# Kernel optimization log

Hardware: AMD Instinct MI355X
Metric: run time of the kernel (lower is better)

The kernel has to match this reference:

```python
import jax, jax.numpy as jnp
import numpy as np

D_MODEL, HEADS, D_FF = 768, 12, 3072
D_K = D_MODEL // HEADS
EPS = 1e-6


def _norm(x, alpha, bias):
    # NormalizationLayer: scalar alpha/bias, torch.std is unbiased (ddof=1)
    mean = jnp.mean(x, axis=-1, keepdims=True)
    std = jnp.std(x, axis=-1, ddof=1, keepdims=True)
    return alpha * (x - mean) / (std + EPS) + bias


def setup_inputs() -> dict:
    key = jax.random.key(0)
    ks = jax.random.split(key, 16)
    B, S = 2, 4096
    x = jax.random.normal(ks[0], (B, S, D_MODEL), dtype=jnp.float32)
    mask = jax.random.randint(ks[1], (B, 1, 1, S), 0, 2, dtype=jnp.int32)
    w = lambda k, o, i: (jax.random.normal(k, (o, i), dtype=jnp.float32) * 0.02)
    return {
        "x": x, "mask": mask,
        "wq": w(ks[2], D_MODEL, D_MODEL), "bq": jnp.zeros((D_MODEL,), jnp.float32),
        "wk": w(ks[3], D_MODEL, D_MODEL), "bk": jnp.zeros((D_MODEL,), jnp.float32),
        "wv": w(ks[4], D_MODEL, D_MODEL), "bv": jnp.zeros((D_MODEL,), jnp.float32),
        "wo": w(ks[5], D_MODEL, D_MODEL), "bo": jnp.zeros((D_MODEL,), jnp.float32),
        "w1": w(ks[6], D_FF, D_MODEL), "b1": jnp.zeros((D_FF,), jnp.float32),
        "w2": w(ks[7], D_MODEL, D_FF), "b2": jnp.zeros((D_MODEL,), jnp.float32),
        "alpha1": jnp.ones((1,), jnp.float32), "beta1": jnp.ones((1,), jnp.float32),
        "alpha2": jnp.ones((1,), jnp.float32), "beta2": jnp.ones((1,), jnp.float32),
    }


def reference(x, mask, wq, bq, wk, bk, wv, bv, wo, bo, w1, b1, w2, b2,
              alpha1, beta1, alpha2, beta2):
    B, S, _ = x.shape

    # --- residual connection 0: pre-norm + self-attention ---
    h = _norm(x, alpha1, beta1)
    q = (h @ wq.T + bq).reshape(B, S, HEADS, D_K).transpose(0, 2, 1, 3)  # [B,H,S,dk]
    k = (h @ wk.T + bk).reshape(B, S, HEADS, D_K).transpose(0, 2, 1, 3)
    v = (h @ wv.T + bv).reshape(B, S, HEADS, D_K).transpose(0, 2, 1, 3)
    scores = jnp.einsum('bhqd,bhkd->bhqk', q, k) / jnp.sqrt(jnp.float32(D_K))
    scores = jnp.where(mask == 0, jnp.float32(-1e9), scores)
    attn = jax.nn.softmax(scores, axis=-1)
    ctx = jnp.einsum('bhqk,bhkd->bhqd', attn, v)
    ctx = ctx.transpose(0, 2, 1, 3).reshape(B, S, D_MODEL)
    x = x + (ctx @ wo.T + bo)

    # --- residual connection 1: pre-norm + FFN ---
    h = _norm(x, alpha2, beta2)
    ff = jax.nn.relu(h @ w1.T + b1) @ w2.T + b2
    return x + ff
```

## Files before the change

kernel.cpp:

```cpp
#include <hip/hip_runtime.h>
#include <hip/hip_bf16.h>
#include <math.h>


typedef __hip_bfloat16 bf16;
typedef short short8 __attribute__((ext_vector_type(8)));
typedef short short4v __attribute__((ext_vector_type(4)));
typedef float f32x4 __attribute__((ext_vector_type(4)));

#define MFMA(A, B, C) __builtin_amdgcn_mfma_f32_16x16x32_bf16(A, B, C, 0, 0, 0)

#if __has_builtin(__builtin_amdgcn_exp2f)
#define EXP2(x) __builtin_amdgcn_exp2f(x)
#else
#define EXP2(x) exp2f(x)
#endif

#define PSWAP32(a, b) asm("v_permlane32_swap_b32 %0, %1" : "+v"(a), "+v"(b))
#define PSWAP16(a, b) asm("v_permlane16_swap_b32 %0, %1" : "+v"(a), "+v"(b))

__device__ __forceinline__ unsigned cvt_pk(float lo, float hi) {
  unsigned r;
  asm("v_cvt_pk_bf16_f32 %0, %1, %2" : "=v"(r) : "v"(lo), "v"(hi));
  return r;
}

__device__ __forceinline__ void gl_lds16(const void* g, void* l) {
  __builtin_amdgcn_global_load_lds(
      (__attribute__((address_space(1))) void*)g,
      (__attribute__((address_space(3))) void*)l, 16, 0, 0);
}

__device__ __forceinline__ short f2b(float f) {
  bf16 h = __float2bfloat16(f);
  return *reinterpret_cast<short*>(&h);
}

__global__ __launch_bounds__(256)
void prep_all(const float* __restrict__ wq, const float* __restrict__ wk,
              const float* __restrict__ wv, const float* __restrict__ wo,
              const float* __restrict__ w1, const float* __restrict__ w2,
              const float* __restrict__ bq, const float* __restrict__ bk,
              const float* __restrict__ bv, const int* __restrict__ mask,
              bf16* __restrict__ wqkvb, bf16* __restrict__ wob,
              bf16* __restrict__ w1b, bf16* __restrict__ w2b,
              float* __restrict__ bqkv,
              int* __restrict__ pos_g, int* __restrict__ nch_g,
              bf16* __restrict__ kc, bf16* __restrict__ vtc)
{
  const int t = threadIdx.x;
  if (blockIdx.x < 2) {
    const int b = blockIdx.x;
    const int* mb = mask + b * 4096;
    __shared__ int lsum[256];
    int loc = 0;
    int mv[16];
#pragma unroll
    for (int j = 0; j < 16; j++) { mv[j] = mb[t * 16 + j] ? 1 : 0; loc += mv[j]; }
    lsum[t] = loc;
    __syncthreads();
    for (int off = 1; off < 256; off <<= 1) {
      int v = (t >= off) ? lsum[t - off] : 0;
      __syncthreads();
      lsum[t] += v;
      __syncthreads();
    }
    const int nvalid = lsum[255];
    int base = lsum[t] - loc;
#pragma unroll
    for (int j = 0; j < 16; j++) {
      pos_g[b * 4096 + t * 16 + j] = mv[j] ? base : -1;
      if (mv[j]) base++;
    }
    const int npad = (nvalid + 63) & ~63;
    if (t == 0) { nch_g[b * 2] = npad >> 6; nch_g[b * 2 + 1] = npad - nvalid; }
    const int npv = npad - nvalid;
    if (npv > 0) {
      const int krows = 12 * npv;
      const short8 z = {};
      for (int task = t; task < krows * 8; task += 256) {
        const int rr = task >> 3, cc = task & 7;
        const int hh = rr / npv, r = nvalid + rr % npv;
        *(short8*)&kc[(((long)(b * 12 + hh) * 4096) + r) * 64 + cc * 8] = z;
      }
      const int vrows = 12 * 64;
      for (int task = t; task < vrows * npv; task += 256) {
        const int row = task / npv, j = nvalid + task % npv;
        const int hh = row >> 6, d = row & 63;
        vtc[((long)((b * 12 + hh) * 64 + d)) * 4096 + j] = __float2bfloat16(0.f);
      }
    }
    return;
  }
  const int i = (blockIdx.x - 2) * 256 + t;
  const int W = 147456;
  const int F = 589824;
  const float* src; bf16* dst; int off;
  if (i < W)          { src = wq; dst = wqkvb;           off = i; }
  else if (i < 2*W)   { src = wk; dst = wqkvb + 589824;  off = i - W; }
  else if (i < 3*W)   { src = wv; dst = wqkvb + 1179648; off = i - 2*W; }
  else if (i < 4*W)   { src = wo; dst = wob;             off = i - 3*W; }
  else if (i < 4*W+F) { src = w1; dst = w1b;             off = i - 4*W; }
  else                { src = w2; dst = w2b;             off = i - 4*W - F; }
  float4 v = ((const float4*)src)[off];
  short4v o;
  o.x = f2b(v.x); o.y = f2b(v.y); o.z = f2b(v.z); o.w = f2b(v.w);
  ((short4v*)dst)[off] = o;
  if (i < 2304)
    bqkv[i] = (i < 768) ? bq[i] : (i < 1536 ? bk[i - 768] : bv[i - 1536]);
}

template<typename INT>
__global__ __launch_bounds__(256)
void ln_kernel(const INT* __restrict__ x, bf16* __restrict__ out,
               const float* __restrict__ alpha, const float* __restrict__ beta)
{
  const int row = blockIdx.x;
  const long base = (long)row * 768;
  const int t = threadIdx.x;
  float v[3]; float s = 0.f, ss = 0.f;
#pragma unroll
  for (int i = 0; i < 3; i++) {
    v[i] = (float)x[base + t + i * 256];
    s += v[i]; ss += v[i] * v[i];
  }
#pragma unroll
  for (int off = 32; off > 0; off >>= 1) {
    s  += __shfl_down(s, off);
    ss += __shfl_down(ss, off);
  }
  __shared__ float red[8];
  __shared__ float stats[2];
  const int w = t >> 6;
  if ((t & 63) == 0) { red[w] = s; red[4 + w] = ss; }
  __syncthreads();
  if (t == 0) {
    float S  = red[0] + red[1] + red[2] + red[3];
    float SS = red[4] + red[5] + red[6] + red[7];
    float mean = S * (1.f / 768.f);
    float var = fmaxf((SS - 768.f * mean * mean) * (1.f / 767.f), 0.f);
    stats[0] = mean;
    stats[1] = 1.f / (sqrtf(var) + 1e-6f);
  }
  __syncthreads();
  const float mean = stats[0], rinv = stats[1];
  const float a = alpha[0], b = beta[0];
#pragma unroll
  for (int i = 0; i < 3; i++)
    out[base + t + i * 256] = __float2bfloat16(a * (v[i] - mean) * rinv + b);
}

template<int MODE, int TM, typename RT, typename OUTT>
__global__ __launch_bounds__(256)
void gemm_bt(const bf16* __restrict__ A, const bf16* __restrict__ W,
             const float* __restrict__ bias, const RT* __restrict__ R,
             OUTT* __restrict__ Cout, int M, int N, int K)
{
  constexpr int MI = TM / 32;
  __shared__ __align__(16) bf16 sA[2][TM * 32];
  __shared__ __align__(16) bf16 sB[2][128 * 32];
  const int t = threadIdx.x;
  const int w = t >> 6, lane = t & 63;
  const int lr = lane & 15, quad = lane >> 4;
  const int tm = blockIdx.x * TM, tn = blockIdx.y * 128;
  const int wm = (w >> 1) * (MI * 16), wn = (w & 1) * 64;

  const int srow = w * 16 + (lane >> 2);
  const int sq = lane & 3;
  const int scol = (sq ^ ((srow >> 1) & 3)) * 8;
  const int soff = srow * 32 + sq * 8;
  const bf16* Ap = A + (long)(tm + srow) * K + scol;
  const bf16* Wp = W + (long)(tn + srow) * K + scol;
  const long half = (long)64 * K;

  auto stage = [&](int kb, int bi) {
    gl_lds16(Ap + kb, &sA[bi][soff]);
    if (TM == 128) gl_lds16(Ap + kb + half, &sA[bi][soff + 64 * 32]);
    gl_lds16(Wp + kb, &sB[bi][soff]);
    gl_lds16(Wp + kb + half, &sB[bi][soff + 64 * 32]);
  };

  const int cQ = (quad ^ ((lr >> 1) & 3)) * 8;

  f32x4 acc[MI][4] = {};

  stage(0, 0);
  int bi = 0;
  for (int kb = 0; kb < K; kb += 32, bi ^= 1) {
    __syncthreads();
    if (kb + 32 < K) stage(kb + 32, bi ^ 1);
    const bf16* sAb = sA[bi];
    const bf16* sBb = sB[bi];
    short8 af[MI], bfr[4];
#pragma unroll
    for (int i = 0; i < MI; i++)
      af[i] = *(const short8*)&sAb[(wm + i * 16 + lr) * 32 + cQ];
#pragma unroll
    for (int j = 0; j < 4; j++)
      bfr[j] = *(const short8*)&sBb[(wn + j * 16 + lr) * 32 + cQ];
#pragma unroll
    for (int i = 0; i < MI; i++)
#pragma unroll
      for (int j = 0; j < 4; j++)
        acc[i][j] = MFMA(af[i], bfr[j], acc[i][j]);
  }

#pragma unroll
  for (int i = 0; i < MI; i++) {
#pragma unroll
    for (int j = 0; j < 4; j++) {
      const int col = tn + wn + j * 16 + lr;
      const float bv = bias[col];
#pragma unroll
      for (int r = 0; r < 4; r++) {
        const int m = tm + wm + i * 16 + quad * 4 + r;
        float vv = acc[i][j][r] + bv;
        if (MODE == 1) vv = fmaxf(vv, 0.f);
        if (MODE == 4) vv += (float)R[(long)m * N + col];
        Cout[(long)m * N + col] = (OUTT)vv;
      }
    }
  }
}

__global__ __launch_bounds__(256)
void gemm_qkv(const bf16* __restrict__ A, const bf16* __restrict__ W,
              const float* __restrict__ bias, const int* __restrict__ pos_g,
              bf16* __restrict__ Qo, bf16* __restrict__ Kc, bf16* __restrict__ Vtc)
{
  const int K = 768;
  __shared__ __align__(16) bf16 sA[2][128 * 32];
  __shared__ __align__(16) bf16 sB[2][128 * 32];
  const int t = threadIdx.x;
  const int w = t >> 6, lane = t & 63;
  const int lr = lane & 15, quad = lane >> 4;
  const int tm = blockIdx.x * 128, tn = blockIdx.y * 128;
  const int wm = (w >> 1) * 64, wn = (w & 1) * 64;

  const int srow = w * 16 + (lane >> 2);
  const int sq = lane & 3;
  const int scol = (sq ^ ((srow >> 1) & 3)) * 8;
  const int soff = srow * 32 + sq * 8;
  const bf16* Ap = A + (long)(tm + srow) * K + scol;
  const bf16* Wp = W + (long)(tn + srow) * K + scol;
  const long half = (long)64 * K;

  auto stage = [&](int kb, int bi) {
    gl_lds16(Ap + kb, &sA[bi][soff]);
    gl_lds16(Ap + kb + half, &sA[bi][soff + 64 * 32]);
    gl_lds16(Wp + kb, &sB[bi][soff]);
    gl_lds16(Wp + kb + half, &sB[bi][soff + 64 * 32]);
  };

  const int cQ = (quad ^ ((lr >> 1) & 3)) * 8;

  f32x4 acc[4][4] = {};

  stage(0, 0);
  int bi = 0;
  for (int kb = 0; kb < K; kb += 32, bi ^= 1) {
    __syncthreads();
    if (kb + 32 < K) stage(kb + 32, bi ^ 1);
    const bf16* sAb = sA[bi];
    const bf16* sBb = sB[bi];
    short8 af[4], bfr[4];
#pragma unroll
    for (int i = 0; i < 4; i++)
      af[i] = *(const short8*)&sAb[(wm + i * 16 + lr) * 32 + cQ];
#pragma unroll
    for (int j = 0; j < 4; j++)
      bfr[j] = *(const short8*)&sBb[(wn + j * 16 + lr) * 32 + cQ];
#pragma unroll
    for (int i = 0; i < 4; i++)
#pragma unroll
      for (int j = 0; j < 4; j++)
        acc[i][j] = MFMA(af[i], bfr[j], acc[i][j]);
  }

  const int region = (tn >= 1536) ? 2 : (tn >= 768 ? 1 : 0);
#pragma unroll
  for (int i = 0; i < 4; i++) {
#pragma unroll
    for (int j = 0; j < 4; j++) {
      const int col = tn + wn + j * 16 + lr;
      const int c768 = col - region * 768;
      const int hh = c768 >> 6, d = c768 & 63;
      const float bv = bias[col];
#pragma unroll
      for (int r = 0; r < 4; r++) {
        const int m = tm + wm + i * 16 + quad * 4 + r;
        const int bb = m >> 12, sdx = m & 4095;
        float vv = acc[i][j][r] + bv;
        if (region == 0) {
          vv *= 0.18033688011112042f;
          Qo[((long)(bb * 12 + hh) * 4096 + sdx) * 64 + d] = __float2bfloat16(vv);
        } else {
          const int p_ = pos_g[bb * 4096 + sdx];
          if (p_ >= 0) {
            if (region == 1)
              Kc[((long)(bb * 12 + hh) * 4096 + p_) * 64 + d] = __float2bfloat16(vv);
            else
              Vtc[((long)(bb * 12 + hh) * 64 + d) * 4096 + p_] = __float2bfloat16(vv);
          }
        }
      }
    }
  }
}

__global__ __launch_bounds__(256)
void attn_kernel(const bf16* __restrict__ Q, const bf16* __restrict__ Kg,
                 const bf16* __restrict__ Vt,
                 const int* __restrict__ nch_g, bf16* __restrict__ ctx)
{
  __shared__ __align__(16) bf16 sK[2][64 * 64];
  __shared__ __align__(16) bf16 sV[2][64 * 64];

  const int t = threadIdx.x, w = t >> 6, lane = t & 63;
  const int lr = lane & 15, quad = lane >> 4;
  const int bh = blockIdx.y, b = bh / 12, hh = bh % 12;
  const int qb = blockIdx.x * 128 + w * 32;
  const long bh_s = (long)bh * 4096;
  const int nch = nch_g[b * 2];
  const int npv = nch_g[b * 2 + 1];

  short8 qf[2][2];
#pragma unroll
  for (int qt = 0; qt < 2; qt++) {
    const bf16* qp = Q + (bh_s + qb + qt * 16 + lr) * 64 + quad * 8;
    qf[qt][0] = *(const short8*)qp;
    qf[qt][1] = *(const short8*)(qp + 32);
  }

  short8 ones;
#pragma unroll
  for (int i = 0; i < 8; i++) ones[i] = (short)0x3F80;

  const int rA = w * 16 + (lane >> 3), rB = rA + 8;
  const int c8 = lane & 7;
  const bf16* kA = Kg + (bh_s + rA) * 64 + ((c8 ^ (rA & 7)) << 3);
  const bf16* kB = Kg + (bh_s + rB) * 64 + ((c8 ^ (rB & 7)) << 3);
  const bf16* vA = Vt + ((long)bh * 64 + rA) * 4096 + ((c8 ^ (rA & 7)) << 3);
  const bf16* vB = Vt + ((long)bh * 64 + rB) * 4096 + ((c8 ^ (rB & 7)) << 3);
  const int ldsA = (w * 16) * 64 + lane * 8;
  const int ldsB = ldsA + 8 * 64;

  const int cA = (quad * 8) ^ ((lr & 7) << 3);

  f32x4 lacc[2] = {};
  f32x4 Ot[4][2] = {};

  auto stage = [&](int kc, int buf) {
    gl_lds16(kA + (long)kc * 64, &sK[buf][ldsA]);
    gl_lds16(kB + (long)kc * 64, &sK[buf][ldsB]);
    gl_lds16(vA + kc, &sV[buf][ldsA]);
    gl_lds16(vB + kc, &sV[buf][ldsB]);
  };

  auto compute = [&](int buf) {
    const bf16* Kb = sK[buf];
    const bf16* Vb = sV[buf];
    f32x4 st[4][2] = {};
    __builtin_amdgcn_s_setprio(1);
#pragma unroll
    for (int kt = 0; kt < 4; kt++) {
      const int rowb = (kt * 16 + lr) * 64;
      short8 kfa = *(const short8*)&Kb[rowb + cA];
      short8 kfb = *(const short8*)&Kb[rowb + (cA ^ 32)];
      st[kt][0] = MFMA(kfa, qf[0][0], st[kt][0]);
      st[kt][0] = MFMA(kfb, qf[0][1], st[kt][0]);
      st[kt][1] = MFMA(kfa, qf[1][0], st[kt][1]);
      st[kt][1] = MFMA(kfb, qf[1][1], st[kt][1]);
    }
    __builtin_amdgcn_s_setprio(0);

    short8 pf[2][2];
#pragma unroll
    for (int qt = 0; qt < 2; qt++) {
      float p[4][4];
#pragma unroll
      for (int kt = 0; kt < 4; kt++)
#pragma unroll
        for (int r = 0; r < 4; r++)
          p[kt][r] = EXP2(st[kt][qt][r]);
      unsigned u00 = cvt_pk(p[0][0], p[0][1]), u01 = cvt_pk(p[0][2], p[0][3]);
      unsigned u10 = cvt_pk(p[1][0], p[1][1]), u11 = cvt_pk(p[1][2], p[1][3]);
      unsigned u20 = cvt_pk(p[2][0], p[2][1]), u21 = cvt_pk(p[2][2], p[2][3]);
      unsigned u30 = cvt_pk(p[3][0], p[3][1]), u31 = cvt_pk(p[3][2], p[3][3]);
      PSWAP32(u00, u10); PSWAP32(u01, u11);
      PSWAP32(u20, u30); PSWAP32(u21, u31);
      PSWAP16(u00, u10); PSWAP16(u01, u11);
      PSWAP16(u20, u30); PSWAP16(u21, u31);
      union { unsigned u[4]; short8 s8; } fa, fb;
      fa.u[0] = u00; fa.u[1] = u01; fa.u[2] = u10; fa.u[3] = u11;
      fb.u[0] = u20; fb.u[1] = u21; fb.u[2] = u30; fb.u[3] = u31;
      pf[qt][0] = fa.s8;
      pf[qt][1] = fb.s8;
    }

    __builtin_amdgcn_s_setprio(1);
#pragma unroll
    for (int dt = 0; dt < 4; dt++) {
      const int rowb = (dt * 16 + lr) * 64;
      short8 vfa = *(const short8*)&Vb[rowb + cA];
      short8 vfb = *(const short8*)&Vb[rowb + (cA ^ 32)];
      Ot[dt][0] = MFMA(vfa, pf[0][0], Ot[dt][0]);
      Ot[dt][0] = MFMA(vfb, pf[0][1], Ot[dt][0]);
      Ot[dt][1] = MFMA(vfa, pf[1][0], Ot[dt][1]);
      Ot[dt][1] = MFMA(vfb, pf[1][1], Ot[dt][1]);
    }
    lacc[0] = MFMA(ones, pf[0][0], lacc[0]);
    lacc[0] = MFMA(ones, pf[0][1], lacc[0]);
    lacc[1] = MFMA(ones, pf[1][0], lacc[1]);
    lacc[1] = MFMA(ones, pf[1][1], lacc[1]);
    __builtin_amdgcn_s_setprio(0);
  };

  stage(0, 0);
  for (int ci = 0; ci < nch; ci++) {
    __syncthreads();
    if (ci + 1 < nch) stage((ci + 1) * 64, (ci + 1) & 1);
    compute(ci & 1);
  }

#pragma unroll
  for (int qt = 0; qt < 2; qt++) {
    const float l = lacc[qt][0] - (float)npv;
    const float il = (l > 0.f) ? 1.f / l : 0.f;
    const int q = qb + qt * 16 + lr;
    bf16* cp = ctx + ((long)(b * 4096 + q)) * 768 + hh * 64 + quad * 4;
#pragma unroll
    for (int dt = 0; dt < 4; dt++) {
      short4v ov;
      ov.x = f2b(Ot[dt][qt][0] * il);
      ov.y = f2b(Ot[dt][qt][1] * il);
      ov.z = f2b(Ot[dt][qt][2] * il);
      ov.w = f2b(Ot[dt][qt][3] * il);
      *(short4v*)(cp + dt * 16) = ov;
    }
  }
}

extern "C" void kernel_launch(void* const* d_in, const int* in_sizes, int n_in,
                              void* d_out, int out_size, void* d_ws, size_t ws_size,
                              hipStream_t stream)
{
  (void)in_sizes; (void)n_in; (void)out_size; (void)ws_size;
  const float* x    = (const float*)d_in[0];
  const int*   mask = (const int*)  d_in[1];
  const float* wq = (const float*)d_in[2];  const float* bq = (const float*)d_in[3];
  const float* wk = (const float*)d_in[4];  const float* bk = (const float*)d_in[5];
  const float* wv = (const float*)d_in[6];  const float* bv = (const float*)d_in[7];
  const float* wo = (const float*)d_in[8];  const float* bo = (const float*)d_in[9];
  const float* w1 = (const float*)d_in[10]; const float* b1 = (const float*)d_in[11];
  const float* w2 = (const float*)d_in[12]; const float* b2 = (const float*)d_in[13];
  const float* alpha1 = (const float*)d_in[14]; const float* beta1 = (const float*)d_in[15];
  const float* alpha2 = (const float*)d_in[16]; const float* beta2 = (const float*)d_in[17];
  float* out = (float*)d_out;

  const long WSZ = (long)768 * 768 * 2;
  const long W1SZ = (long)3072 * 768 * 2;
  const long SZB = (long)8192 * 768 * 2;
  char* ws = (char*)d_ws;
  bf16* wqkvb = (bf16*)(ws);
  bf16* wob = (bf16*)(ws + 3 * WSZ);
  bf16* w1b = (bf16*)(ws + 4 * WSZ);
  bf16* w2b = (bf16*)(ws + 4 * WSZ + W1SZ);
  char* aux = ws + 4 * WSZ + 2 * W1SZ;
  float* bqkv   = (float*)(aux);
  int*   pos_g  = (int*)(aux + 16384);
  int*   nch_g  = (int*)(aux + 81920);
  const long BASE = 16l << 20;
  bf16* h   = (bf16*)(ws + BASE);
  bf16* qws = (bf16*)(ws + BASE + 1 * SZB);
  bf16* kcw = (bf16*)(ws + BASE + 2 * SZB);
  bf16* vtc = (bf16*)(ws + BASE + 3 * SZB);
  bf16* ctx = (bf16*)(ws + BASE + 4 * SZB);
  bf16* x1  = (bf16*)(ws + BASE + 5 * SZB);
  bf16* ff  = qws;

  dim3 blk(256);

  hipLaunchKernelGGL(prep_all, dim3(6914), blk, 0, stream,
                     wq, wk, wv, wo, w1, w2, bq, bk, bv, mask,
                     wqkvb, wob, w1b, w2b, bqkv, pos_g, nch_g, kcw, vtc);

  hipLaunchKernelGGL((ln_kernel<float>), dim3(8192), blk, 0, stream, x, h, alpha1, beta1);
  hipLaunchKernelGGL(gemm_qkv, dim3(64, 18), blk, 0, stream, h, wqkvb, bqkv, pos_g, qws, kcw, vtc);
  hipLaunchKernelGGL(attn_kernel, dim3(32, 24), blk, 0, stream, qws, kcw, vtc, nch_g, ctx);
  hipLaunchKernelGGL((gemm_bt<4, 64, float, bf16>), dim3(128, 6), blk, 0, stream, ctx, wob, bo, x, x1, 8192, 768, 768);
  hipLaunchKernelGGL((ln_kernel<bf16>), dim3(8192), blk, 0, stream, x1, h, alpha2, beta2);
  hipLaunchKernelGGL((gemm_bt<1, 128, float, bf16>), dim3(64, 24), blk, 0, stream, h, w1b, b1, (const float*)nullptr, ff, 8192, 3072, 768);
  hipLaunchKernelGGL((gemm_bt<4, 64, bf16, float>), dim3(128, 6), blk, 0, stream, ff, w2b, b2, x1, out, 8192, 768, 3072);
}
```

Before: 400.2 us.

## Software-pipeline attention loop: overlap next QK^T with current softmax-PV

Splits the per-chunk attention compute into a QK^T stage and a softmax+PV stage, and issues the QK^T MFMAs for chunk i+1 before the exp/PV work of chunk i. K/V staging moves from a double buffer to a triple buffer so the in-flight tile stays valid. The aim is to interleave the exp/convert VALU work with independent MFMA work and hide the matrix-unit latency. In exchange it uses more LDS per block and more registers for two score buffers, which could reduce occupancy.

Measured after the change: 461.2 us. +15.3%, slower.

```diff
diff --git a/kernel.cpp b/kernel.cpp
--- a/kernel.cpp
+++ b/kernel.cpp
@@ -313,8 +313,8 @@
                  const bf16* __restrict__ Vt,
                  const int* __restrict__ nch_g, bf16* __restrict__ ctx)
 {
-  __shared__ __align__(16) bf16 sK[2][64 * 64];
-  __shared__ __align__(16) bf16 sV[2][64 * 64];
+  __shared__ __align__(16) bf16 sK[3][64 * 64];
+  __shared__ __align__(16) bf16 sV[3][64 * 64];
 
   const int t = threadIdx.x, w = t >> 6, lane = t & 63;
   const int lr = lane & 15, quad = lane >> 4;
@@ -350,30 +350,32 @@
   f32x4 lacc[2] = {};
   f32x4 Ot[4][2] = {};
 
-  auto stage = [&](int kc, int buf) {
-    gl_lds16(kA + (long)kc * 64, &sK[buf][ldsA]);
-    gl_lds16(kB + (long)kc * 64, &sK[buf][ldsB]);
-    gl_lds16(vA + kc, &sV[buf][ldsA]);
-    gl_lds16(vB + kc, &sV[buf][ldsB]);
+  auto stage = [&](int kc, int s) {
+    gl_lds16(kA + (long)kc * 64, &sK[s][ldsA]);
+    gl_lds16(kB + (long)kc * 64, &sK[s][ldsB]);
+    gl_lds16(vA + kc, &sV[s][ldsA]);
+    gl_lds16(vB + kc, &sV[s][ldsB]);
   };
 
-  auto compute = [&](int buf) {
-    const bf16* Kb = sK[buf];
-    const bf16* Vb = sV[buf];
-    f32x4 st[4][2] = {};
+  auto qk = [&](int s, f32x4 (&st)[4][2]) {
+    const bf16* Kb = sK[s];
     __builtin_amdgcn_s_setprio(1);
 #pragma unroll
     for (int kt = 0; kt < 4; kt++) {
       const int rowb = (kt * 16 + lr) * 64;
       short8 kfa = *(const short8*)&Kb[rowb + cA];
       short8 kfb = *(const short8*)&Kb[rowb + (cA ^ 32)];
+      st[kt][0] = {}; st[kt][1] = {};
       st[kt][0] = MFMA(kfa, qf[0][0], st[kt][0]);
       st[kt][0] = MFMA(kfb, qf[0][1], st[kt][0]);
       st[kt][1] = MFMA(kfa, qf[1][0], st[kt][1]);
       st[kt][1] = MFMA(kfb, qf[1][1], st[kt][1]);
     }
     __builtin_amdgcn_s_setprio(0);
-
+  };
+
+  auto sm_pv = [&](int s, f32x4 (&st)[4][2]) {
+    const bf16* Vb = sV[s];
     short8 pf[2][2];
 #pragma unroll
     for (int qt = 0; qt < 2; qt++) {
@@ -416,11 +418,31 @@
     __builtin_amdgcn_s_setprio(0);
   };
 
+  f32x4 stA[4][2], stB[4][2];
+
   stage(0, 0);
-  for (int ci = 0; ci < nch; ci++) {
+  __syncthreads();
+  if (nch > 1) stage(64, 1);
+  if (nch > 0) qk(0, stA);
+
+  int ci = 0;
+  while (ci + 1 < nch) {
     __syncthreads();
-    if (ci + 1 < nch) stage((ci + 1) * 64, (ci + 1) & 1);
-    compute(ci & 1);
+    if (ci + 2 < nch) stage((ci + 2) * 64, (ci + 2) % 3);
+    qk((ci + 1) % 3, stB);
+    sm_pv(ci % 3, stA);
+    ci++;
+    if (ci + 1 >= nch) break;
+    __syncthreads();
+    if (ci + 2 < nch) stage((ci + 2) * 64, (ci + 2) % 3);
+    qk((ci + 1) % 3, stA);
+    sm_pv(ci % 3, stB);
+    ci++;
+  }
+  if (ci < nch) {
+    __syncthreads();
+    if (ci & 1) sm_pv(ci % 3, stB);
+    else        sm_pv(ci % 3, stA);
   }
 
 #pragma unroll
```
